# Kernel optimization log

Hardware: AMD Instinct MI355X
Metric: run time of the kernel (lower is better)

The kernel has to match this reference:

```python
import jax, jax.numpy as jnp
import numpy as np

B, T, J, D = 32, 1024, 256, 512

def setup_inputs() -> dict:
    key = jax.random.key(0)
    k1, k2, k3 = jax.random.split(key, 3)
    h = jax.random.normal(k1, (B, T, D), dtype=jnp.float32)
    u = jax.random.normal(k2, (B, J, D), dtype=jnp.float32)
    w = jax.random.normal(k3, (1, 3 * D), dtype=jnp.float32) * 0.05
    return {"h": h, "u": u, "w": w}

def reference(h, u, w):
    # S[b,i,j] = w . concat([h_i, u_j, h_i*u_j])
    # Algebraic decomposition: w = [w_h, w_u, w_m]
    d = h.shape[-1]
    w = w[0]
    w_h, w_u, w_m = w[:d], w[d:2*d], w[2*d:]
    # [B,T,1] + [B,1,J] + [B,T,J]
    term_h = jnp.einsum('btd,d->bt', h, w_h)[:, :, None]
    term_u = jnp.einsum('bjd,d->bj', u, w_u)[:, None, :]
    term_m = jnp.einsum('btd,bjd->btj', h * w_m, u)
    return term_h + term_u + term_m
```

## Files before the change

### kernel.cpp

```cpp
#include <hip/hip_runtime.h>
#include <hip/hip_bf16.h>
#include <stdint.h>

#define B_ 32
#define T_ 1024
#define J_ 256
#define D_ 512

typedef __attribute__((ext_vector_type(8))) short short8;
typedef __attribute__((ext_vector_type(4))) float floatx4;

__global__ __launch_bounds__(256) void prep_u_kernel(
    const float* __restrict__ u, const float* __restrict__ w,
    __hip_bfloat16* __restrict__ B2, float* __restrict__ tu)
{
    int row  = blockIdx.x * 4 + (threadIdx.x >> 6);
    int lane = threadIdx.x & 63;
    const float* src = u + (size_t)row * D_;
    int base = lane * 8;

    float4 v0  = *(const float4*)(src + base);
    float4 v1  = *(const float4*)(src + base + 4);
    float4 wh0 = *(const float4*)(w + base);
    float4 wh1 = *(const float4*)(w + base + 4);
    float4 wu0 = *(const float4*)(w + D_ + base);
    float4 wu1 = *(const float4*)(w + D_ + base + 4);
    float4 wm0 = *(const float4*)(w + 2*D_ + base);
    float4 wm1 = *(const float4*)(w + 2*D_ + base + 4);

    float s = v0.x*wu0.x + v0.y*wu0.y + v0.z*wu0.z + v0.w*wu0.w
            + v1.x*wu1.x + v1.y*wu1.y + v1.z*wu1.z + v1.w*wu1.w;

    float vals[8] = {
        v0.x*wm0.x + wh0.x, v0.y*wm0.y + wh0.y,
        v0.z*wm0.z + wh0.z, v0.w*wm0.w + wh0.w,
        v1.x*wm1.x + wh1.x, v1.y*wm1.y + wh1.y,
        v1.z*wm1.z + wh1.z, v1.w*wm1.w + wh1.w };

    union { __hip_bfloat16 b[8]; uint4 q; } pk;
#pragma unroll
    for (int i = 0; i < 8; i++) pk.b[i] = __float2bfloat16(vals[i]);
    *(uint4*)(B2 + (size_t)row * D_ + base) = pk.q;

#pragma unroll
    for (int off = 32; off > 0; off >>= 1) s += __shfl_down(s, off, 64);
    if (lane == 0) tu[row] = s;
}

__device__ inline void gload_lds16(const void* g, void* l) {
    __builtin_amdgcn_global_load_lds(
        (__attribute__((address_space(1))) void*)(g),
        (__attribute__((address_space(3))) void*)(l),
        16, 0, 0);
}

__global__ __launch_bounds__(256) void gemm_kernel(
    const float* __restrict__ h,
    const __hip_bfloat16* __restrict__ B2,
    const float* __restrict__ tu,
    float* __restrict__ out)
{
    __shared__ __align__(16) __hip_bfloat16 sA[128 * 32];
    __shared__ __align__(16) __hip_bfloat16 sB[128 * 32];

    const int b   = blockIdx.y;
    const int tM  = blockIdx.x >> 1;
    const int tN  = blockIdx.x & 1;
    const int tid = threadIdx.x;
    const int w = tid >> 6, lane = tid & 63;
    const int wr = w >> 1, wc = w & 1;

    const float*          Ah = h  + ((size_t)b * T_ + tM * 128) * D_;
    const __hip_bfloat16* Bb = B2 + ((size_t)b * J_ + tN * 128) * D_;

    const int sr = tid >> 2;
    const int sc = (tid & 3) * 8;
    const int ldsOffB = tid * 8;

    const int ar = tid >> 1;
    const int ac = (tid & 1) * 16;

    floatx4 acc[4][4];
#pragma unroll
    for (int i = 0; i < 4; i++)
#pragma unroll
        for (int j = 0; j < 4; j++) acc[i][j] = (floatx4)0.0f;

    const int kb = (lane >> 4) * 8;
    const int fr = lane & 15;

    for (int k0 = 0; k0 < D_; k0 += 32) {
        gload_lds16(Bb + (size_t)sr        * D_ + k0 + sc, sB + ldsOffB);
        gload_lds16(Bb + (size_t)(sr + 64) * D_ + k0 + sc, sB + 64 * 32 + ldsOffB);

        {
            const float* ap = Ah + (size_t)ar * D_ + k0 + ac;
            float4 a0 = *(const float4*)(ap);
            float4 a1 = *(const float4*)(ap + 4);
            float4 a2 = *(const float4*)(ap + 8);
            float4 a3 = *(const float4*)(ap + 12);
            union { __hip_bfloat16 b[16]; uint4 q[2]; } pk;
            pk.b[0]=__float2bfloat16(a0.x); pk.b[1]=__float2bfloat16(a0.y);
            pk.b[2]=__float2bfloat16(a0.z); pk.b[3]=__float2bfloat16(a0.w);
            pk.b[4]=__float2bfloat16(a1.x); pk.b[5]=__float2bfloat16(a1.y);
            pk.b[6]=__float2bfloat16(a1.z); pk.b[7]=__float2bfloat16(a1.w);
            pk.b[8]=__float2bfloat16(a2.x); pk.b[9]=__float2bfloat16(a2.y);
            pk.b[10]=__float2bfloat16(a2.z); pk.b[11]=__float2bfloat16(a2.w);
            pk.b[12]=__float2bfloat16(a3.x); pk.b[13]=__float2bfloat16(a3.y);
            pk.b[14]=__float2bfloat16(a3.z); pk.b[15]=__float2bfloat16(a3.w);
            uint4* dst = (uint4*)(sA + ar * 32 + ac);
            dst[0] = pk.q[0];
            dst[1] = pk.q[1];
        }
        __syncthreads();

        short8 af[4], bfr[4];
#pragma unroll
        for (int mi = 0; mi < 4; mi++)
            af[mi] = *(const short8*)(sA + (wr * 64 + mi * 16 + fr) * 32 + kb);
#pragma unroll
        for (int ni = 0; ni < 4; ni++)
            bfr[ni] = *(const short8*)(sB + (wc * 64 + ni * 16 + fr) * 32 + kb);
#pragma unroll
        for (int mi = 0; mi < 4; mi++)
#pragma unroll
            for (int ni = 0; ni < 4; ni++)
                acc[mi][ni] = __builtin_amdgcn_mfma_f32_16x16x32_bf16(
                    af[mi], bfr[ni], acc[mi][ni], 0, 0, 0);
        __syncthreads();
    }

    const size_t outB = (size_t)b * T_ * J_;
    const int colq = lane & 15;
    const int rq   = (lane >> 4) * 4;
    const float* tub = tu + b * J_;
#pragma unroll
    for (int mi = 0; mi < 4; mi++) {
        int r0 = tM * 128 + wr * 64 + mi * 16 + rq;
#pragma unroll
        for (int ni = 0; ni < 4; ni++) {
            int col = tN * 128 + wc * 64 + ni * 16 + colq;
            float tuv = tub[col];
#pragma unroll
            for (int r = 0; r < 4; r++) {
                out[outB + (size_t)(r0 + r) * J_ + col] =
                    acc[mi][ni][r] + tuv;
            }
        }
    }
}

extern "C" void kernel_launch(void* const* d_in, const int* in_sizes, int n_in,
                              void* d_out, int out_size, void* d_ws, size_t ws_size,
                              hipStream_t stream)
{
    const float* h = (const float*)d_in[0];
    const float* u = (const float*)d_in[1];
    const float* w = (const float*)d_in[2];
    float* out = (float*)d_out;

    uint8_t* ws = (uint8_t*)d_ws;
    __hip_bfloat16* B2 = (__hip_bfloat16*)ws;
    float* tu = (float*)(ws + (size_t)B_ * J_ * D_ * 2);

    prep_u_kernel<<<dim3(B_ * J_ / 4), 256, 0, stream>>>(u, w, B2, tu);

    gemm_kernel<<<dim3((T_ / 128) * (J_ / 128), B_), 256, 0, stream>>>(h, B2, tu, out);
}
```

Baseline: 136.6 us.

## Halve GEMM M-tile to 64 rows and XOR-swizzle LDS layout

Shrinks the per-block M tile from 128 to 64 rows, doubling the grid to 1024 blocks so more blocks are resident across CUs, and cuts per-warp accumulators from 16 to 8 MFMA tiles. Both A and B tiles in LDS now use an XOR swizzle on the 16-byte column chunk, applied at store time and undone at fragment-read time, to reduce LDS bank conflicts. The cost is that each B tile is loaded twice as often from global memory and each block does less MFMA work per barrier.

```diff
diff --git a/kernel.cpp b/kernel.cpp
--- a/kernel.cpp
+++ b/kernel.cpp
@@ -60,7 +60,7 @@
     const float* __restrict__ tu,
     float* __restrict__ out)
 {
-    __shared__ __align__(16) __hip_bfloat16 sA[128 * 32];
+    __shared__ __align__(16) __hip_bfloat16 sA[64 * 32];
     __shared__ __align__(16) __hip_bfloat16 sB[128 * 32];
 
     const int b   = blockIdx.y;
@@ -70,59 +70,53 @@
     const int w = tid >> 6, lane = tid & 63;
     const int wr = w >> 1, wc = w & 1;
 
-    const float*          Ah = h  + ((size_t)b * T_ + tM * 128) * D_;
+    const float*          Ah = h  + ((size_t)b * T_ + tM * 64) * D_;
     const __hip_bfloat16* Bb = B2 + ((size_t)b * J_ + tN * 128) * D_;
 
-    const int sr = tid >> 2;
-    const int sc = (tid & 3) * 8;
-    const int ldsOffB = tid * 8;
+    const int srow = tid >> 2;
+    const int scb  = ((tid & 3) ^ ((tid >> 3) & 3));
+    const int ssc  = scb * 8;
+    const int ldsOff = tid * 8;
 
-    const int ar = tid >> 1;
-    const int ac = (tid & 1) * 16;
-
-    floatx4 acc[4][4];
+    floatx4 acc[2][4];
 #pragma unroll
-    for (int i = 0; i < 4; i++)
+    for (int i = 0; i < 2; i++)
 #pragma unroll
         for (int j = 0; j < 4; j++) acc[i][j] = (floatx4)0.0f;
 
-    const int kb = (lane >> 4) * 8;
+    const int cb = lane >> 4;
     const int fr = lane & 15;
 
     for (int k0 = 0; k0 < D_; k0 += 32) {
-        gload_lds16(Bb + (size_t)sr        * D_ + k0 + sc, sB + ldsOffB);
-        gload_lds16(Bb + (size_t)(sr + 64) * D_ + k0 + sc, sB + 64 * 32 + ldsOffB);
+        gload_lds16(Bb + (size_t)srow        * D_ + k0 + ssc, sB + ldsOff);
+        gload_lds16(Bb + (size_t)(srow + 64) * D_ + k0 + ssc, sB + 64 * 32 + ldsOff);
 
         {
-            const float* ap = Ah + (size_t)ar * D_ + k0 + ac;
+            const float* ap = Ah + (size_t)srow * D_ + k0 + ssc;
             float4 a0 = *(const float4*)(ap);
             float4 a1 = *(const float4*)(ap + 4);
-            float4 a2 = *(const float4*)(ap + 8);
-            float4 a3 = *(const float4*)(ap + 12);
-            union { __hip_bfloat16 b[16]; uint4 q[2]; } pk;
+            union { __hip_bfloat16 b[8]; uint4 q; } pk;
             pk.b[0]=__float2bfloat16(a0.x); pk.b[1]=__float2bfloat16(a0.y);
             pk.b[2]=__float2bfloat16(a0.z); pk.b[3]=__float2bfloat16(a0.w);
             pk.b[4]=__float2bfloat16(a1.x); pk.b[5]=__float2bfloat16(a1.y);
             pk.b[6]=__float2bfloat16(a1.z); pk.b[7]=__float2bfloat16(a1.w);
-            pk.b[8]=__float2bfloat16(a2.x); pk.b[9]=__float2bfloat16(a2.y);
-            pk.b[10]=__float2bfloat16(a2.z); pk.b[11]=__float2bfloat16(a2.w);
-            pk.b[12]=__float2bfloat16(a3.x); pk.b[13]=__float2bfloat16(a3.y);
-            pk.b[14]=__float2bfloat16(a3.z); pk.b[15]=__float2bfloat16(a3.w);
-            uint4* dst = (uint4*)(sA + ar * 32 + ac);
-            dst[0] = pk.q[0];
-            dst[1] = pk.q[1];
+            *(uint4*)(sA + ldsOff) = pk.q;
         }
         __syncthreads();
 
-        short8 af[4], bfr[4];
+        short8 af[2], bfr[4];
 #pragma unroll
-        for (int mi = 0; mi < 4; mi++)
-            af[mi] = *(const short8*)(sA + (wr * 64 + mi * 16 + fr) * 32 + kb);
+        for (int mi = 0; mi < 2; mi++) {
+            int rr = wr * 32 + mi * 16 + fr;
+            af[mi] = *(const short8*)(sA + rr * 32 + ((cb ^ ((rr >> 1) & 3)) << 3));
+        }
 #pragma unroll
-        for (int ni = 0; ni < 4; ni++)
-            bfr[ni] = *(const short8*)(sB + (wc * 64 + ni * 16 + fr) * 32 + kb);
+        for (int ni = 0; ni < 4; ni++) {
+            int rr = wc * 64 + ni * 16 + fr;
+            bfr[ni] = *(const short8*)(sB + rr * 32 + ((cb ^ ((rr >> 1) & 3)) << 3));
+        }
 #pragma unroll
-        for (int mi = 0; mi < 4; mi++)
+        for (int mi = 0; mi < 2; mi++)
 #pragma unroll
             for (int ni = 0; ni < 4; ni++)
                 acc[mi][ni] = __builtin_amdgcn_mfma_f32_16x16x32_bf16(
@@ -135,8 +129,8 @@
     const int rq   = (lane >> 4) * 4;
     const float* tub = tu + b * J_;
 #pragma unroll
-    for (int mi = 0; mi < 4; mi++) {
-        int r0 = tM * 128 + wr * 64 + mi * 16 + rq;
+    for (int mi = 0; mi < 2; mi++) {
+        int r0 = tM * 64 + wr * 32 + mi * 16 + rq;
 #pragma unroll
         for (int ni = 0; ni < 4; ni++) {
             int col = tN * 128 + wc * 64 + ni * 16 + colq;
@@ -165,5 +159,5 @@
 
     prep_u_kernel<<<dim3(B_ * J_ / 4), 256, 0, stream>>>(u, w, B2, tu);
 
-    gemm_kernel<<<dim3((T_ / 128) * (J_ / 128), B_), 256, 0, stream>>>(h, B2, tu, out);
+    gemm_kernel<<<dim3((T_ / 64) * (J_ / 128), B_), 256, 0, stream>>>(h, B2, tu, out);
 }
```

New measurement: 139.5 us. 1.02x slower.
